# Performance work log

Hardware: AMD Instinct MI355X
Metric: run time of the kernel (lower is better)

Reference implementation:

```python
import jax, jax.numpy as jnp
import numpy as np

N_NODES = 100000
N_TRIPLES = 2000000
HIDDEN = 48


def setup_inputs() -> dict:
    key = jax.random.key(0)
    k = jax.random.split(key, 8)
    h = jax.random.normal(k[0], (N_NODES, HIDDEN), dtype=jnp.float32)
    tb_index = jax.random.randint(k[1], (N_TRIPLES, 3), 0, N_NODES, dtype=jnp.int64)
    tb_d1 = jax.random.uniform(k[2], (N_TRIPLES,), dtype=jnp.float32)
    tb_d2 = jax.random.uniform(k[3], (N_TRIPLES,), dtype=jnp.float32)
    W3 = jax.random.normal(k[4], (HIDDEN, HIDDEN), dtype=jnp.float32) / np.sqrt(HIDDEN)
    Wu = jax.random.normal(k[5], (HIDDEN, 2 * HIDDEN), dtype=jnp.float32) / np.sqrt(2 * HIDDEN)
    gamma = jnp.ones((HIDDEN,), dtype=jnp.float32)
    beta = jnp.zeros((HIDDEN,), dtype=jnp.float32)
    return {"h": h, "tb_index": tb_index, "tb_d1": tb_d1, "tb_d2": tb_d2,
            "W3": W3, "Wu": Wu, "gamma": gamma, "beta": beta}


def _layernorm(x, gamma, beta, eps=1e-5):
    mu = jnp.mean(x, axis=-1, keepdims=True)
    var = jnp.mean(jnp.square(x - mu), axis=-1, keepdims=True)
    return (x - mu) * jax.lax.rsqrt(var + eps) * gamma + beta


def reference(h, tb_index, tb_d1, tb_d2, W3, Wu, gamma, beta):
    center = tb_index[:, 0]
    nb1 = tb_index[:, 1]
    nb2 = tb_index[:, 2]
    N = h.shape[0]
    # per-triple scalar weight from distance asymmetry
    asym = jnp.abs(tb_d1 - tb_d2) / (jnp.maximum(tb_d1, tb_d2) + 1e-8)
    weight = 1.0 + 0.3 * asym                                   # [T]
    # gather -> small GEMM: msg = W_3body(h[nb1] + h[nb2])
    msg = jnp.einsum('th,oh->to', h[nb1] + h[nb2], W3)          # [T, H]
    combined = jnp.concatenate([h[center], msg], axis=-1)       # [T, 2H]
    pre = jnp.einsum('tc,oc->to', combined, Wu)                 # [T, H]
    delta = jnp.where(pre > 0, pre, 0.01 * pre) * weight[:, None]
    # scatter-add with count normalization
    nc = jax.ops.segment_sum(jnp.ones_like(weight), center, num_segments=N)
    nc = jnp.maximum(nc, 1.0)                                   # [N]
    agg = jax.ops.segment_sum(delta, center, num_segments=N)    # [N, H]
    agg = agg / jnp.sqrt(nc)[:, None]
    return _layernorm(h + agg, gamma, beta)
```

## Files before the change

kernel.cpp:

```cpp
#include <hip/hip_runtime.h>
#include <hip/hip_bf16.h>
#include <hip/hip_fp16.h>
#include <stdint.h>

#define NN 100000
#define NT 2000000
#define HD 48
#define VS 64
#define CAP 56
#define NPB 20
#define NBH ((NT + 255) / 256)
#define NB ((NN + 1023) / 1024)

#define BINB 64
#define NBIN ((NN + BINB - 1) / BINB)
#define BINCAP 1792
#define CHK 8192
#define NCHK ((NT + CHK - 1) / CHK)
#define TPT (CHK / 1024)
#define NNODEB (NN / NPB)
#define FATGRID (NCHK + NNODEB)

#define WSCALE (1.3f / 32767.0f)
#define WQUANT (32767.0f / 1.3f)

typedef _Float16 hf2 __attribute__((ext_vector_type(2)));

__device__ __forceinline__ float b2f(__hip_bfloat16 x) { return __bfloat162float(x); }

__device__ __forceinline__ float ldf(const void* p, long long i, int isbf16) {
    if (isbf16) return b2f(((const __hip_bfloat16*)p)[i]);
    return ((const float*)p)[i];
}

__device__ __forceinline__ hf2 habs2(hf2 x) {
    union { hf2 h; unsigned int u; } c; c.h = x; c.u &= 0x7FFF7FFFu; return c.h;
}
__device__ __forceinline__ hf2 splat2(float f) {
    hf2 r; r.x = (_Float16)f; r.y = (_Float16)f; return r;
}
union V4H { uint4 u; hf2 h[4]; };

__global__ __launch_bounds__(256) void prep_kernel(
        const unsigned int* __restrict__ hw, const unsigned int* __restrict__ iw,
        int* __restrict__ flags,
        const void* __restrict__ W3, const void* __restrict__ Wu,
        float* __restrict__ wu1f, float* __restrict__ bf,
        int* __restrict__ gcur) {
    __shared__ int cbf, cix;
    int tid = threadIdx.x;
    if (tid == 0) { cbf = 0; cix = 0; }
    __syncthreads();
    unsigned int e = (hw[tid] >> 7) & 0xff;
    if (e >= 90 && e <= 144) atomicAdd(&cbf, 1);
    if (blockIdx.x == 0 && iw[2 * tid + 1] == 0) atomicAdd(&cix, 1);
    __syncthreads();
    int fb = (cbf >= 192) ? 1 : 0;
    if (blockIdx.x == 0 && tid == 0) {
        flags[0] = fb;
        flags[1] = (cix >= 255) ? 1 : 0;
    }
    for (int i = blockIdx.x * 256 + tid; i < NBIN * 32; i += 9 * 256)
        gcur[i] = 0;
    int i = blockIdx.x * 256 + tid;
    if (i < HD * HD) {
        int o = i / HD, hh = i % HD;
        wu1f[i] = ldf(Wu, o * 2 * HD + hh, fb);
        float s = 0.f;
        #pragma unroll 8
        for (int k = 0; k < HD; ++k)
            s += ldf(Wu, o * 2 * HD + HD + k, fb) * ldf(W3, k * HD + hh, fb);
        bf[i] = s;
    }
}

struct NodeLds { float Ws[HD * 49]; float Bs[HD * 49]; float hs[NPB * HD]; };
struct BinLds  { int h1[NBIN]; int h2[NBIN]; int gb[NBIN]; };
union FatLds   { NodeLds n; BinLds b; };

__global__ __launch_bounds__(1024, 2) void fused_nb_kernel(
        const void* __restrict__ h, const int* __restrict__ flags,
        const float* __restrict__ wu1f, const float* __restrict__ bf,
        __half* __restrict__ uh, __half* __restrict__ vh,
        const void* __restrict__ idxp,
        const void* __restrict__ d1p, const void* __restrict__ d2p,
        int* __restrict__ gcur, uint2* __restrict__ binned) {
    __shared__ FatLds L;
    int tid = threadIdx.x;
    int fb = flags[0];

    if (blockIdx.x < NCHK) {
        int fi = flags[1];
        for (int i = tid; i < NBIN; i += 1024) { L.b.h1[i] = 0; L.b.h2[i] = 0; }
        __syncthreads();
        int t0 = blockIdx.x * CHK;
        const int* qi = (const int*)idxp;

        unsigned mx[TPT], my[TPT];
        int bn[TPT];
        #pragma unroll
        for (int j = 0; j < TPT; ++j) {
            int t = t0 + j * 1024 + tid;
            if (t < NT) {
                int c, n1, n2;
                if (fi) {
                    c  = qi[6LL * t];
                    n1 = qi[6LL * t + 2];
                    n2 = qi[6LL * t + 4];
                } else {
                    c  = qi[3LL * t];
                    n1 = qi[3LL * t + 1];
                    n2 = qi[3LL * t + 2];
                }
                float d1 = ldf(d1p, t, fb);
                float d2 = ldf(d2p, t, fb);
                float asym = fabsf(d1 - d2) / (fmaxf(d1, d2) + 1e-8f);
                unsigned qw = (unsigned)((1.0f + 0.3f * asym) * WQUANT + 0.5f);
                if (qw > 32767u) qw = 32767u;
                bn[j] = c >> 6;
                mx[j] = (unsigned)n1 | (qw << 17);
                my[j] = (unsigned)n2 | ((unsigned)(c & 63) << 17);
                atomicAdd(&L.b.h1[bn[j]], 1);
            } else {
                bn[j] = -1;
            }
        }
        __syncthreads();
        for (int b = tid; b < NBIN; b += 1024) {
            int n = L.b.h1[b];
            L.b.gb[b] = n ? atomicAdd(&gcur[b << 5], n) : 0;
        }
        __syncthreads();
        #pragma unroll
        for (int j = 0; j < TPT; ++j) {
            if (bn[j] >= 0) {
                int r = atomicAdd(&L.b.h2[bn[j]], 1);
                int pos = L.b.gb[bn[j]] + r;
                if (pos < BINCAP)
                    binned[(size_t)bn[j] * BINCAP + pos] = make_uint2(mx[j], my[j]);
            }
        }
    } else {
        int base = (blockIdx.x - NCHK) * NPB;
        for (int i = tid; i < HD * HD; i += 1024) {
            int o = i / HD, hh = i % HD;
            L.n.Ws[o * 49 + hh] = wu1f[i];
            L.n.Bs[o * 49 + hh] = bf[i];
        }
        for (int i = tid; i < NPB * HD; i += 1024)
            L.n.hs[i] = ldf(h, (long long)base * HD + i, fb);
        if (tid < NPB * 16) {
            int ln = tid >> 4, o = HD + (tid & 15);
            vh[(size_t)(base + ln) * VS + o] = (__half)0.f;
        }
        __syncthreads();
        for (int i = tid; i < NPB * HD; i += 1024) {
            int ln = i / HD, o = i - ln * HD;
            const float* hr = L.n.hs + ln * HD;
            const float* wr = L.n.Ws + o * 49;
            const float* br = L.n.Bs + o * 49;
            float su = 0.f, sv = 0.f;
            #pragma unroll
            for (int k = 0; k < HD; ++k) { float hv = hr[k]; su += wr[k] * hv; sv += br[k] * hv; }
            int n = base + ln;
            uh[(size_t)n * HD + o] = __float2half(su);
            vh[(size_t)n * VS + o] = __float2half(sv);
        }
    }
}

__global__ __launch_bounds__(512, 4) void bin_accum_kernel(
        const void* __restrict__ h, const int* __restrict__ flags,
        const __half* __restrict__ uh, const __half* __restrict__ vh,
        const int* __restrict__ gcur, const uint2* __restrict__ binned,
        const void* __restrict__ gamma, const void* __restrict__ beta,
        void* __restrict__ out) {
    __shared__ uint2 buckets[BINB][64];
    __shared__ int   cur[BINB];
    __shared__ float ucs[8][64];
    __shared__ float accs[8][HD];
    int tid = threadIdx.x, fb = flags[0];
    int bin = blockIdx.x;

    for (int i = tid; i < BINB; i += 512) cur[i] = 0;
    __syncthreads();

    int nm = gcur[bin << 5]; if (nm > BINCAP) nm = BINCAP;
    const uint2* bp = binned + (size_t)bin * BINCAP;
    for (int i = tid; i < nm; i += 512) {
        uint2 m = bp[i];
        int cl = (m.y >> 17) & (BINB - 1);
        int r = atomicAdd(&cur[cl], 1);
        if (r < CAP) buckets[cl][r] = m;
    }
    __syncthreads();

    int wv = tid >> 6, lane = tid & 63;
    int s = lane >> 3, dg = lane & 7;
    const char* vb = (const char*)vh;
    size_t dgo = (size_t)dg * 16;
    float gv = (lane < HD) ? ldf(gamma, lane, fb) : 0.f;
    float bv = (lane < HD) ? ldf(beta, lane, fb) : 0.f;

    for (int ci = 0; ci < BINB / 8; ++ci) {
        int cl = wv * (BINB / 8) + ci;
        int n = bin * BINB + cl;
        if (n >= NN) continue;

        int m = cur[cl]; if (m > CAP) m = CAP;
        float hval = (lane < HD) ? ldf(h, (long long)n * HD + lane, fb) : 0.f;
        float uval = (lane < HD) ? __half2float(uh[(size_t)n * HD + lane]) : 0.f;
        ucs[wv][lane] = uval;
        hf2 uc4[4];
        #pragma unroll
        for (int j = 0; j < 4; ++j) {
            uc4[j].x = (_Float16)ucs[wv][dg * 8 + 2 * j];
            uc4[j].y = (_Float16)ucs[wv][dg * 8 + 2 * j + 1];
        }

        float accf[8] = {0.f, 0.f, 0.f, 0.f, 0.f, 0.f, 0.f, 0.f};
        for (int t = 0; t < m; t += 16) {
            uint2 m0 = buckets[cl][t + s];
            uint2 m1 = buckets[cl][t + 8 + s];
            int v0 = (t + s) < m, v1 = (t + 8 + s) < m;
            unsigned a0 = v0 ? (m0.x & 0x1FFFFu) : 0u;
            unsigned b0 = v0 ? (m0.y & 0x1FFFFu) : 0u;
            float w0 = v0 ? (float)(m0.x >> 17) * WSCALE : 0.f;
            unsigned a1 = v1 ? (m1.x & 0x1FFFFu) : 0u;
            unsigned b1 = v1 ? (m1.y & 0x1FFFFu) : 0u;
            float w1 = v1 ? (float)(m1.x >> 17) * WSCALE : 0.f;
            V4H pa0, pb0, pa1, pb1;
            pa0.u = *(const uint4*)(vb + (size_t)a0 * 128 + dgo);
            pb0.u = *(const uint4*)(vb + (size_t)b0 * 128 + dgo);
            pa1.u = *(const uint4*)(vb + (size_t)a1 * 128 + dgo);
            pb1.u = *(const uint4*)(vb + (size_t)b1 * 128 + dgo);
            hf2 aw0 = splat2(0.505f * w0), bw0 = splat2(0.495f * w0);
            hf2 aw1 = splat2(0.505f * w1), bw1 = splat2(0.495f * w1);
            #pragma unroll
            for (int j = 0; j < 4; ++j) {
                hf2 p0 = pa0.h[j] + pb0.h[j] + uc4[j];
                hf2 acch = p0 * aw0 + habs2(p0) * bw0;
                hf2 p1 = pa1.h[j] + pb1.h[j] + uc4[j];
                acch += p1 * aw1 + habs2(p1) * bw1;
                accf[2 * j]     += (float)acch.x;
                accf[2 * j + 1] += (float)acch.y;
            }
        }

        #pragma unroll
        for (int j = 0; j < 8; ++j) {
            accf[j] += __shfl_xor(accf[j], 8, 64);
            accf[j] += __shfl_xor(accf[j], 16, 64);
            accf[j] += __shfl_xor(accf[j], 32, 64);
        }
        if (lane < 6) {
            #pragma unroll
            for (int j = 0; j < 8; ++j) accs[wv][lane * 8 + j] = accf[j];
        }
        float av = (lane < HD) ? accs[wv][lane] : 0.f;

        float rnc = rsqrtf(fmaxf((float)m, 1.0f));
        float x = (lane < HD) ? (hval + av * rnc) : 0.f;
        float su = x, sq = x * x;
        #pragma unroll
        for (int o = 32; o; o >>= 1) {
            su += __shfl_xor(su, o, 64);
            sq += __shfl_xor(sq, o, 64);
        }
        float mu   = su * (1.0f / HD);
        float var  = sq * (1.0f / HD) - mu * mu;
        float rstd = rsqrtf(var + 1e-5f);
        if (lane < HD) {
            float r = (x - mu) * rstd * gv + bv;
            if (fb) ((__hip_bfloat16*)out)[(size_t)n * HD + lane] = __float2bfloat16(r);
            else    ((float*)out)[(size_t)n * HD + lane] = r;
        }
    }
}

__global__ __launch_bounds__(256) void node_kernel(
        const void* __restrict__ h, const int* __restrict__ flags,
        const float* __restrict__ wu1f, const float* __restrict__ bf,
        __half* __restrict__ uh, __half* __restrict__ vh) {
    __shared__ float Ws[HD * 49];
    __shared__ float Bs[HD * 49];
    __shared__ float hs[16 * HD];
    int tid = threadIdx.x;
    int fb = flags[0];
    for (int i = tid; i < HD * HD; i += 256) {
        int o = i / HD, hh = i % HD;
        Ws[o * 49 + hh] = wu1f[i];
        Bs[o * 49 + hh] = bf[i];
    }
    int base = blockIdx.x * 16;
    for (int i = tid; i < 16 * HD; i += 256)
        hs[i] = ldf(h, (long long)base * HD + i, fb);
    {
        int ln = tid >> 4, o = HD + (tid & 15);
        vh[(size_t)(base + ln) * VS + o] = (__half)0.f;
    }
    __syncthreads();
    for (int i = tid; i < 16 * HD; i += 256) {
        int ln = i / HD, o = i - ln * HD;
        const float* hr = hs + ln * HD;
        const float* wr = Ws + o * 49;
        const float* br = Bs + o * 49;
        float su = 0.f, sv = 0.f;
        #pragma unroll
        for (int k = 0; k < HD; ++k) { float hv = hr[k]; su += wr[k] * hv; sv += br[k] * hv; }
        int n = base + ln;
        uh[(size_t)n * HD + o] = __float2half(su);
        vh[(size_t)n * VS + o] = __float2half(sv);
    }
}

__global__ __launch_bounds__(256) void hist_kernel(const void* __restrict__ idxp,
                                                   const int* __restrict__ flags,
                                                   int* __restrict__ cnt) {
    int t = blockIdx.x * 256 + threadIdx.x;
    if (t >= NT) return;
    int c = flags[1] ? (int)((const long long*)idxp)[3LL * t]
                     : ((const int*)idxp)[3 * t];
    atomicAdd(&cnt[c << 4], 1);
}

__global__ __launch_bounds__(1024) void scan_part(const int* __restrict__ cnt,
                                                  int* __restrict__ off,
                                                  int* __restrict__ bsum) {
    __shared__ int wsums[16];
    int tid = threadIdx.x, lane = tid & 63, wv = tid >> 6;
    int i = blockIdx.x * 1024 + tid;
    int x = (i < NN) ? cnt[i << 4] : 0;
    int vx = x;
    #pragma unroll
    for (int o = 1; o < 64; o <<= 1) {
        int y = __shfl_up(vx, o, 64);
        if (lane >= o) vx += y;
    }
    if (lane == 63) wsums[wv] = vx;
    __syncthreads();
    if (tid == 0) {
        int s = 0;
        #pragma unroll
        for (int k = 0; k < 16; ++k) { int t2 = wsums[k]; wsums[k] = s; s += t2; }
        bsum[blockIdx.x] = s;
    }
    __syncthreads();
    if (i < NN) off[i] = wsums[wv] + vx - x;
}

__global__ __launch_bounds__(1024) void scan_add(int* __restrict__ off,
                                                 const int* __restrict__ bsum) {
    int bid = blockIdx.x;
    int pre = 0;
    for (int k = 0; k < bid; ++k) pre += bsum[k];
    int i = bid * 1024 + threadIdx.x;
    if (i < NN) off[i] += pre;
}

__global__ __launch_bounds__(256) void scatter_kernel(
        const void* __restrict__ idxp,
        const void* __restrict__ d1p, const void* __restrict__ d2p,
        const int* __restrict__ flags, int* __restrict__ cur,
        uint2* __restrict__ sp) {
    int t = blockIdx.x * 256 + threadIdx.x;
    if (t >= NT) return;
    int fb = flags[0];
    int c, n1, n2;
    if (flags[1]) {
        const long long* q = (const long long*)idxp;
        c = (int)q[3LL * t]; n1 = (int)q[3LL * t + 1]; n2 = (int)q[3LL * t + 2];
    } else {
        const int* q = (const int*)idxp;
        c = q[3 * t]; n1 = q[3 * t + 1]; n2 = q[3 * t + 2];
    }
    float d1 = ldf(d1p, t, fb);
    float d2 = ldf(d2p, t, fb);
    float asym = fabsf(d1 - d2) / (fmaxf(d1, d2) + 1e-8f);
    unsigned int qw = (unsigned int)((1.0f + 0.3f * asym) * WQUANT + 0.5f);
    if (qw > 32767u) qw = 32767u;
    uint2 m = make_uint2((unsigned int)n1 | (qw << 17), (unsigned int)n2);
    int pos = atomicAdd(&cur[c], 1);
    sp[pos] = m;
}

__global__ __launch_bounds__(256) void accum_kernel(
        const void* __restrict__ h, const int* __restrict__ flags,
        const __half* __restrict__ uh, const __half* __restrict__ vh,
        const int* __restrict__ seg, const uint2* __restrict__ sp,
        const void* __restrict__ gamma, const void* __restrict__ beta,
        void* __restrict__ out) {
    __shared__ uint2 metas[4][64];
    __shared__ float ucs[4][64];
    __shared__ float accs[4][HD];
    int tid = threadIdx.x, fb = flags[0];
    int wv = tid >> 6, lane = tid & 63;
    int n = blockIdx.x * 4 + wv;

    float hval = (lane < HD) ? ldf(h, (long long)n * HD + lane, fb) : 0.f;
    float uval = (lane < HD) ? __half2float(uh[(size_t)n * HD + lane]) : 0.f;
    ucs[wv][lane] = uval;

    int s = lane >> 3, dg = lane & 7;
    hf2 uc4[4];
    #pragma unroll
    for (int j = 0; j < 4; ++j) {
        uc4[j].x = (_Float16)ucs[wv][dg * 8 + 2 * j];
        uc4[j].y = (_Float16)ucs[wv][dg * 8 + 2 * j + 1];
    }

    int start = (n == 0) ? 0 : seg[n - 1];
    int end = seg[n];
    float accf[8] = {0.f, 0.f, 0.f, 0.f, 0.f, 0.f, 0.f, 0.f};
    const char* vb = (const char*)vh;
    size_t dgo = (size_t)dg * 16;

    for (int chunk = start; chunk < end; chunk += 64) {
        int m = end - chunk; if (m > 64) m = 64;
        if (lane < m) metas[wv][lane] = sp[chunk + lane];
        for (int t = 0; t < m; t += 16) {
            uint2 m0 = metas[wv][t + s];
            uint2 m1 = metas[wv][t + 8 + s];
            int v0 = (t + s) < m, v1 = (t + 8 + s) < m;
            unsigned a0 = v0 ? (m0.x & 0x1FFFFu) : 0u;
            unsigned b0 = v0 ? (m0.y & 0x1FFFFu) : 0u;
            float w0 = v0 ? (float)(m0.x >> 17) * WSCALE : 0.f;
            unsigned a1 = v1 ? (m1.x & 0x1FFFFu) : 0u;
            unsigned b1 = v1 ? (m1.y & 0x1FFFFu) : 0u;
            float w1 = v1 ? (float)(m1.x >> 17) * WSCALE : 0.f;
            V4H pa0, pb0, pa1, pb1;
            pa0.u = *(const uint4*)(vb + (size_t)a0 * 128 + dgo);
            pb0.u = *(const uint4*)(vb + (size_t)b0 * 128 + dgo);
            pa1.u = *(const uint4*)(vb + (size_t)a1 * 128 + dgo);
            pb1.u = *(const uint4*)(vb + (size_t)b1 * 128 + dgo);
            hf2 aw0 = splat2(0.505f * w0), bw0 = splat2(0.495f * w0);
            hf2 aw1 = splat2(0.505f * w1), bw1 = splat2(0.495f * w1);
            #pragma unroll
            for (int j = 0; j < 4; ++j) {
                hf2 p0 = pa0.h[j] + pb0.h[j] + uc4[j];
                hf2 acch = p0 * aw0 + habs2(p0) * bw0;
                hf2 p1 = pa1.h[j] + pb1.h[j] + uc4[j];
                acch += p1 * aw1 + habs2(p1) * bw1;
                accf[2 * j]     += (float)acch.x;
                accf[2 * j + 1] += (float)acch.y;
            }
        }
    }

    #pragma unroll
    for (int j = 0; j < 8; ++j) {
        accf[j] += __shfl_xor(accf[j], 8, 64);
        accf[j] += __shfl_xor(accf[j], 16, 64);
        accf[j] += __shfl_xor(accf[j], 32, 64);
    }
    if (lane < 6) {
        #pragma unroll
        for (int j = 0; j < 8; ++j) accs[wv][lane * 8 + j] = accf[j];
    }
    float av = (lane < HD) ? accs[wv][lane] : 0.f;

    float rnc = rsqrtf(fmaxf((float)(end - start), 1.0f));
    float x = (lane < HD) ? (hval + av * rnc) : 0.f;
    float su = x, sq = x * x;
    #pragma unroll
    for (int o = 32; o; o >>= 1) {
        su += __shfl_xor(su, o, 64);
        sq += __shfl_xor(sq, o, 64);
    }
    float mu   = su * (1.0f / HD);
    float var  = sq * (1.0f / HD) - mu * mu;
    float rstd = rsqrtf(var + 1e-5f);
    if (lane < HD) {
        float g  = ldf(gamma, lane, fb);
        float bb = ldf(beta, lane, fb);
        float r = (x - mu) * rstd * g + bb;
        if (fb) ((__hip_bfloat16*)out)[(size_t)n * HD + lane] = __float2bfloat16(r);
        else    ((float*)out)[(size_t)n * HD + lane] = r;
    }
}

extern "C" void kernel_launch(void* const* d_in, const int* in_sizes, int n_in,
                              void* d_out, int out_size, void* d_ws, size_t ws_size,
                              hipStream_t stream) {
    const void* h     = d_in[0];
    const void* idx   = d_in[1];
    const void* d1    = d_in[2];
    const void* d2    = d_in[3];
    const void* W3    = d_in[4];
    const void* Wu    = d_in[5];
    const void* gamma = d_in[6];
    const void* beta  = d_in[7];

    char* base  = (char*)d_ws;
    int*   flags = (int*)base;
    float* wu1f  = (float*)(base + 64);
    float* bf    = wu1f + HD * HD;
    uintptr_t ua = (uintptr_t)(bf + HD * HD);
    __half* uh   = (__half*)((ua + 127) & ~(uintptr_t)127);
    __half* vh   = (__half*)((char*)uh + (size_t)NN * HD * 2);
    char*  after = (char*)vh + (size_t)NN * VS * 2;

    int*   gcur = (int*)after;
    uintptr_t bna = (uintptr_t)(gcur + (size_t)NBIN * 32);
    uint2* binned = (uint2*)((bna + 127) & ~(uintptr_t)127);
    size_t need_primary = ((char*)(binned + (size_t)NBIN * BINCAP)) - base;

    int*   cnt  = (int*)after;
    int*   off  = (int*)(cnt + (size_t)NN * 16);
    int*   bsum = off + NN;
    uintptr_t spa = (uintptr_t)(bsum + 256);
    uint2* sp   = (uint2*)((spa + 15) & ~(uintptr_t)15);

    prep_kernel<<<(HD * HD + 255) / 256, 256, 0, stream>>>(
        (const unsigned int*)h, (const unsigned int*)idx, flags, W3, Wu,
        wu1f, bf, gcur);

    if (ws_size >= need_primary) {
        fused_nb_kernel<<<FATGRID, 1024, 0, stream>>>(
            h, flags, wu1f, bf, uh, vh, idx, d1, d2, gcur, binned);
        bin_accum_kernel<<<NBIN, 512, 0, stream>>>(h, flags, uh, vh, gcur, binned,
                                                   gamma, beta, d_out);
    } else {
        node_kernel<<<NN / 16, 256, 0, stream>>>(h, flags, wu1f, bf, uh, vh);
        hipMemsetAsync(cnt, 0, (size_t)NN * 16 * sizeof(int), stream);
        hist_kernel<<<NBH, 256, 0, stream>>>(idx, flags, cnt);
        scan_part<<<NB, 1024, 0, stream>>>(cnt, off, bsum);
        scan_add<<<NB, 1024, 0, stream>>>(off, bsum);
        scatter_kernel<<<(NT + 255) / 256, 256, 0, stream>>>(
            idx, d1, d2, flags, off, sp);
        accum_kernel<<<NN / 4, 256, 0, stream>>>(h, flags, uh, vh, off, sp,
                                                 gamma, beta, d_out);
    }
}
```

Before: 261.1 us.

## Bin triples into 256-node superbins with direct global atomics

The binning phase no longer builds a per-block LDS histogram with a reserve-then-scatter pass. Each triple now takes a slot with a global atomicAdd into one of about 391 superbins of 256 nodes, cutting bins per kernel fourfold. The accumulate kernel keeps one block per 64-node bin, so each block now reads the whole superbin (up to 6144 entries) and filters out the quarter that belongs to it. This trades away two syncthreads and the LDS histogram work for heavy global atomic contention on few counters and four times the binned-buffer reads in the accumulate stage.

```diff
diff --git a/kernel.cpp b/kernel.cpp
--- a/kernel.cpp
+++ b/kernel.cpp
@@ -14,10 +14,11 @@
 
 #define BINB 64
 #define NBIN ((NN + BINB - 1) / BINB)
-#define BINCAP 1792
+#define SBB 256
+#define NSB ((NN + SBB - 1) / SBB)
+#define SBCAP 6144
 #define CHK 8192
 #define NCHK ((NT + CHK - 1) / CHK)
-#define TPT (CHK / 1024)
 #define NNODEB (NN / NPB)
 #define FATGRID (NCHK + NNODEB)
 
@@ -60,7 +61,7 @@
         flags[0] = fb;
         flags[1] = (cix >= 255) ? 1 : 0;
     }
-    for (int i = blockIdx.x * 256 + tid; i < NBIN * 32; i += 9 * 256)
+    for (int i = blockIdx.x * 256 + tid; i < NSB * 32; i += 9 * 256)
         gcur[i] = 0;
     int i = blockIdx.x * 256 + tid;
     if (i < HD * HD) {
@@ -74,81 +75,58 @@
     }
 }
 
-struct NodeLds { float Ws[HD * 49]; float Bs[HD * 49]; float hs[NPB * HD]; };
-struct BinLds  { int h1[NBIN]; int h2[NBIN]; int gb[NBIN]; };
-union FatLds   { NodeLds n; BinLds b; };
-
-__global__ __launch_bounds__(1024, 2) void fused_nb_kernel(
+__global__ __launch_bounds__(1024) void fused_nb_kernel(
         const void* __restrict__ h, const int* __restrict__ flags,
         const float* __restrict__ wu1f, const float* __restrict__ bf,
         __half* __restrict__ uh, __half* __restrict__ vh,
         const void* __restrict__ idxp,
         const void* __restrict__ d1p, const void* __restrict__ d2p,
         int* __restrict__ gcur, uint2* __restrict__ binned) {
-    __shared__ FatLds L;
+    __shared__ float Ws[HD * 49];
+    __shared__ float Bs[HD * 49];
+    __shared__ float hs[NPB * HD];
     int tid = threadIdx.x;
     int fb = flags[0];
 
     if (blockIdx.x < NCHK) {
         int fi = flags[1];
-        for (int i = tid; i < NBIN; i += 1024) { L.b.h1[i] = 0; L.b.h2[i] = 0; }
-        __syncthreads();
         int t0 = blockIdx.x * CHK;
         const int* qi = (const int*)idxp;
-
-        unsigned mx[TPT], my[TPT];
-        int bn[TPT];
-        #pragma unroll
-        for (int j = 0; j < TPT; ++j) {
+        #pragma unroll
+        for (int j = 0; j < CHK / 1024; ++j) {
             int t = t0 + j * 1024 + tid;
-            if (t < NT) {
-                int c, n1, n2;
-                if (fi) {
-                    c  = qi[6LL * t];
-                    n1 = qi[6LL * t + 2];
-                    n2 = qi[6LL * t + 4];
-                } else {
-                    c  = qi[3LL * t];
-                    n1 = qi[3LL * t + 1];
-                    n2 = qi[3LL * t + 2];
-                }
-                float d1 = ldf(d1p, t, fb);
-                float d2 = ldf(d2p, t, fb);
-                float asym = fabsf(d1 - d2) / (fmaxf(d1, d2) + 1e-8f);
-                unsigned qw = (unsigned)((1.0f + 0.3f * asym) * WQUANT + 0.5f);
-                if (qw > 32767u) qw = 32767u;
-                bn[j] = c >> 6;
-                mx[j] = (unsigned)n1 | (qw << 17);
-                my[j] = (unsigned)n2 | ((unsigned)(c & 63) << 17);
-                atomicAdd(&L.b.h1[bn[j]], 1);
+            if (t >= NT) continue;
+            int c, n1, n2;
+            if (fi) {
+                c  = qi[6LL * t];
+                n1 = qi[6LL * t + 2];
+                n2 = qi[6LL * t + 4];
             } else {
-                bn[j] = -1;
+                c  = qi[3LL * t];
+                n1 = qi[3LL * t + 1];
+                n2 = qi[3LL * t + 2];
             }
-        }
-        __syncthreads();
-        for (int b = tid; b < NBIN; b += 1024) {
-            int n = L.b.h1[b];
-            L.b.gb[b] = n ? atomicAdd(&gcur[b << 5], n) : 0;
-        }
-        __syncthreads();
-        #pragma unroll
-        for (int j = 0; j < TPT; ++j) {
-            if (bn[j] >= 0) {
-                int r = atomicAdd(&L.b.h2[bn[j]], 1);
-                int pos = L.b.gb[bn[j]] + r;
-                if (pos < BINCAP)
-                    binned[(size_t)bn[j] * BINCAP + pos] = make_uint2(mx[j], my[j]);
-            }
+            float d1 = ldf(d1p, t, fb);
+            float d2 = ldf(d2p, t, fb);
+            float asym = fabsf(d1 - d2) / (fmaxf(d1, d2) + 1e-8f);
+            unsigned qw = (unsigned)((1.0f + 0.3f * asym) * WQUANT + 0.5f);
+            if (qw > 32767u) qw = 32767u;
+            int sb = c >> 8;
+            int r = atomicAdd(&gcur[sb << 5], 1);
+            if (r < SBCAP)
+                binned[(size_t)sb * SBCAP + r] =
+                    make_uint2((unsigned)n1 | (qw << 17),
+                               (unsigned)n2 | ((unsigned)(c & 255) << 17));
         }
     } else {
         int base = (blockIdx.x - NCHK) * NPB;
         for (int i = tid; i < HD * HD; i += 1024) {
             int o = i / HD, hh = i % HD;
-            L.n.Ws[o * 49 + hh] = wu1f[i];
-            L.n.Bs[o * 49 + hh] = bf[i];
+            Ws[o * 49 + hh] = wu1f[i];
+            Bs[o * 49 + hh] = bf[i];
         }
         for (int i = tid; i < NPB * HD; i += 1024)
-            L.n.hs[i] = ldf(h, (long long)base * HD + i, fb);
+            hs[i] = ldf(h, (long long)base * HD + i, fb);
         if (tid < NPB * 16) {
             int ln = tid >> 4, o = HD + (tid & 15);
             vh[(size_t)(base + ln) * VS + o] = (__half)0.f;
@@ -156,9 +134,9 @@
         __syncthreads();
         for (int i = tid; i < NPB * HD; i += 1024) {
             int ln = i / HD, o = i - ln * HD;
-            const float* hr = L.n.hs + ln * HD;
-            const float* wr = L.n.Ws + o * 49;
-            const float* br = L.n.Bs + o * 49;
+            const float* hr = hs + ln * HD;
+            const float* wr = Ws + o * 49;
+            const float* br = Bs + o * 49;
             float su = 0.f, sv = 0.f;
             #pragma unroll
             for (int k = 0; k < HD; ++k) { float hv = hr[k]; su += wr[k] * hv; sv += br[k] * hv; }
@@ -181,17 +159,22 @@
     __shared__ float accs[8][HD];
     int tid = threadIdx.x, fb = flags[0];
     int bin = blockIdx.x;
+    int sb = bin >> 2;
+    unsigned grp = (unsigned)(bin & 3);
 
     for (int i = tid; i < BINB; i += 512) cur[i] = 0;
     __syncthreads();
 
-    int nm = gcur[bin << 5]; if (nm > BINCAP) nm = BINCAP;
-    const uint2* bp = binned + (size_t)bin * BINCAP;
+    int nm = gcur[sb << 5]; if (nm > SBCAP) nm = SBCAP;
+    const uint2* bp = binned + (size_t)sb * SBCAP;
     for (int i = tid; i < nm; i += 512) {
         uint2 m = bp[i];
-        int cl = (m.y >> 17) & (BINB - 1);
-        int r = atomicAdd(&cur[cl], 1);
-        if (r < CAP) buckets[cl][r] = m;
+        unsigned cc = (m.y >> 17) & 255u;
+        if ((cc >> 6) == grp) {
+            int cl = (int)(cc & 63u);
+            int r = atomicAdd(&cur[cl], 1);
+            if (r < CAP) buckets[cl][r] = m;
+        }
     }
     __syncthreads();
 
@@ -501,9 +484,9 @@
     char*  after = (char*)vh + (size_t)NN * VS * 2;
 
     int*   gcur = (int*)after;
-    uintptr_t bna = (uintptr_t)(gcur + (size_t)NBIN * 32);
+    uintptr_t bna = (uintptr_t)(gcur + (size_t)NSB * 32);
     uint2* binned = (uint2*)((bna + 127) & ~(uintptr_t)127);
-    size_t need_primary = ((char*)(binned + (size_t)NBIN * BINCAP)) - base;
+    size_t need_primary = ((char*)(binned + (size_t)NSB * SBCAP)) - base;
 
     int*   cnt  = (int*)after;
     int*   off  = (int*)(cnt + (size_t)NN * 16);
```

Result: slower. 335.8 us (+28.6%).

## Sort binned triples in LDS before writing to global bins for coalescing

Applied to the files above, without the earlier changes.

The binning phase now does a count pass, an LDS exclusive scan over bin counts, and a local counting sort of packed triples in shared memory. It then writes to global bins in sorted order, using a binary search to map each slot back to its bin, so stores to the same bin are contiguous. Chunk size is halved to fit the sorted buffer in LDS, and the launch-bounds occupancy hint is dropped. The cost is re-reading the indices, many scan barriers, and a per-element binary search, plus lower occupancy from the larger LDS footprint.

```diff
diff --git a/kernel.cpp b/kernel.cpp
--- a/kernel.cpp
+++ b/kernel.cpp
@@ -15,9 +15,10 @@
 #define BINB 64
 #define NBIN ((NN + BINB - 1) / BINB)
 #define BINCAP 1792
-#define CHK 8192
+#define CHK 4096
 #define NCHK ((NT + CHK - 1) / CHK)
 #define TPT (CHK / 1024)
+#define SCANN 2048
 #define NNODEB (NN / NPB)
 #define FATGRID (NCHK + NNODEB)
 
@@ -75,10 +76,10 @@
 }
 
 struct NodeLds { float Ws[HD * 49]; float Bs[HD * 49]; float hs[NPB * HD]; };
-struct BinLds  { int h1[NBIN]; int h2[NBIN]; int gb[NBIN]; };
+struct BinLds  { int h1[NBIN]; int gb[NBIN]; int pre[SCANN]; uint2 sorted[CHK]; };
 union FatLds   { NodeLds n; BinLds b; };
 
-__global__ __launch_bounds__(1024, 2) void fused_nb_kernel(
+__global__ __launch_bounds__(1024) void fused_nb_kernel(
         const void* __restrict__ h, const int* __restrict__ flags,
         const float* __restrict__ wu1f, const float* __restrict__ bf,
         __half* __restrict__ uh, __half* __restrict__ vh,
@@ -91,54 +92,82 @@
 
     if (blockIdx.x < NCHK) {
         int fi = flags[1];
-        for (int i = tid; i < NBIN; i += 1024) { L.b.h1[i] = 0; L.b.h2[i] = 0; }
+        for (int i = tid; i < NBIN; i += 1024) L.b.h1[i] = 0;
         __syncthreads();
         int t0 = blockIdx.x * CHK;
         const int* qi = (const int*)idxp;
 
-        unsigned mx[TPT], my[TPT];
-        int bn[TPT];
         #pragma unroll
         for (int j = 0; j < TPT; ++j) {
             int t = t0 + j * 1024 + tid;
             if (t < NT) {
-                int c, n1, n2;
-                if (fi) {
-                    c  = qi[6LL * t];
-                    n1 = qi[6LL * t + 2];
-                    n2 = qi[6LL * t + 4];
-                } else {
-                    c  = qi[3LL * t];
-                    n1 = qi[3LL * t + 1];
-                    n2 = qi[3LL * t + 2];
-                }
-                float d1 = ldf(d1p, t, fb);
-                float d2 = ldf(d2p, t, fb);
-                float asym = fabsf(d1 - d2) / (fmaxf(d1, d2) + 1e-8f);
-                unsigned qw = (unsigned)((1.0f + 0.3f * asym) * WQUANT + 0.5f);
-                if (qw > 32767u) qw = 32767u;
-                bn[j] = c >> 6;
-                mx[j] = (unsigned)n1 | (qw << 17);
-                my[j] = (unsigned)n2 | ((unsigned)(c & 63) << 17);
-                atomicAdd(&L.b.h1[bn[j]], 1);
+                int c = fi ? qi[6LL * t] : qi[3LL * t];
+                atomicAdd(&L.b.h1[c >> 6], 1);
+            }
+        }
+        __syncthreads();
+        for (int b = tid; b < SCANN; b += 1024) {
+            int cnt = (b < NBIN) ? L.b.h1[b] : 0;
+            L.b.pre[b] = cnt;
+            if (b < NBIN) {
+                L.b.gb[b] = cnt ? atomicAdd(&gcur[b << 5], cnt) : 0;
+                L.b.h1[b] = 0;
+            }
+        }
+        __syncthreads();
+        for (int d = 1; d < SCANN; d <<= 1) {
+            int i2 = (tid + 1) * (d << 1) - 1;
+            if (i2 < SCANN) L.b.pre[i2] += L.b.pre[i2 - d];
+            __syncthreads();
+        }
+        if (tid == 0) L.b.pre[SCANN - 1] = 0;
+        __syncthreads();
+        for (int d = SCANN >> 1; d >= 1; d >>= 1) {
+            int i2 = (tid + 1) * (d << 1) - 1;
+            if (i2 < SCANN) {
+                int tmp = L.b.pre[i2 - d];
+                L.b.pre[i2 - d] = L.b.pre[i2];
+                L.b.pre[i2] += tmp;
+            }
+            __syncthreads();
+        }
+        #pragma unroll
+        for (int j = 0; j < TPT; ++j) {
+            int t = t0 + j * 1024 + tid;
+            if (t >= NT) continue;
+            int c, n1, n2;
+            if (fi) {
+                c  = qi[6LL * t];
+                n1 = qi[6LL * t + 2];
+                n2 = qi[6LL * t + 4];
             } else {
-                bn[j] = -1;
-            }
+                c  = qi[3LL * t];
+                n1 = qi[3LL * t + 1];
+                n2 = qi[3LL * t + 2];
+            }
+            float d1 = ldf(d1p, t, fb);
+            float d2 = ldf(d2p, t, fb);
+            float asym = fabsf(d1 - d2) / (fmaxf(d1, d2) + 1e-8f);
+            unsigned qw = (unsigned)((1.0f + 0.3f * asym) * WQUANT + 0.5f);
+            if (qw > 32767u) qw = 32767u;
+            int bn = c >> 6;
+            int rk = atomicAdd(&L.b.h1[bn], 1);
+            L.b.sorted[L.b.pre[bn] + rk] =
+                make_uint2((unsigned)n1 | (qw << 17),
+                           (unsigned)n2 | ((unsigned)(c & 63) << 17));
         }
         __syncthreads();
-        for (int b = tid; b < NBIN; b += 1024) {
-            int n = L.b.h1[b];
-            L.b.gb[b] = n ? atomicAdd(&gcur[b << 5], n) : 0;
-        }
-        __syncthreads();
-        #pragma unroll
-        for (int j = 0; j < TPT; ++j) {
-            if (bn[j] >= 0) {
-                int r = atomicAdd(&L.b.h2[bn[j]], 1);
-                int pos = L.b.gb[bn[j]] + r;
-                if (pos < BINCAP)
-                    binned[(size_t)bn[j] * BINCAP + pos] = make_uint2(mx[j], my[j]);
-            }
+        int total = L.b.pre[NBIN];
+        for (int i = tid; i < total; i += 1024) {
+            int lo = 0, hi = NBIN - 1;
+            while (lo < hi) {
+                int mid = (lo + hi + 1) >> 1;
+                if (L.b.pre[mid] <= i) lo = mid; else hi = mid - 1;
+            }
+            int rk = i - L.b.pre[lo];
+            int pos = L.b.gb[lo] + rk;
+            if (pos < BINCAP)
+                binned[(size_t)lo * BINCAP + pos] = L.b.sorted[i];
         }
     } else {
         int base = (blockIdx.x - NCHK) * NPB;
```

New measurement: 277.1 us. 6.2% more time.
